# Performance work log

Measured on AMD Instinct MI355X. Metric: run time of the kernel, lower is better.

## Reference

```python
import jax, jax.numpy as jnp
import numpy as np

N_HEADS = 6
N_KV_HEADS = 2
HEAD_DIM = 128
REPEATS = N_HEADS // N_KV_HEADS  # 3


def setup_inputs() -> dict:
    key = jax.random.key(0)
    ks = jax.random.split(key, 5)
    B, S, D = 2, 4096, 768
    std = 1.0 / np.sqrt(D)
    return {
        "x": jax.random.normal(ks[0], (B, S, D), dtype=jnp.float32),
        "wq": jax.random.normal(ks[1], (D, N_HEADS * HEAD_DIM), dtype=jnp.float32) * std,
        "wk": jax.random.normal(ks[2], (D, N_KV_HEADS * HEAD_DIM), dtype=jnp.float32) * std,
        "wv": jax.random.normal(ks[3], (D, N_KV_HEADS * HEAD_DIM), dtype=jnp.float32) * std,
        "wo": jax.random.normal(ks[4], (N_HEADS * HEAD_DIM, D), dtype=jnp.float32) * std,
    }


def reference(x, wq, wk, wv, wo):
    B, S, _ = x.shape
    # projections
    q = (x @ wq).reshape(B, S, N_HEADS, HEAD_DIM)
    k = (x @ wk).reshape(B, S, N_KV_HEADS, HEAD_DIM)
    v = (x @ wv).reshape(B, S, N_KV_HEADS, HEAD_DIM)
    # GQA: repeat kv heads (repeat_interleave along head axis)
    k = jnp.repeat(k, REPEATS, axis=2)  # [B,S,H,D]
    v = jnp.repeat(v, REPEATS, axis=2)
    scale = 1.0 / jnp.sqrt(jnp.asarray(HEAD_DIM, x.dtype))
    # full bidirectional attention, [B,H,S,S] scores
    attn = jnp.einsum("bqhd,bkhd->bhqk", q * scale, k)
    attn = jax.nn.softmax(attn, axis=-1)
    out = jnp.einsum("bhqk,bkhd->bqhd", attn, v).reshape(B, S, N_HEADS * HEAD_DIM)
    return out @ wo
```

## Files before the change

### kernel.cpp

```cpp
#include <hip/hip_runtime.h>


typedef __attribute__((ext_vector_type(8))) short bf16x8;
typedef __attribute__((ext_vector_type(4))) float floatx4;
typedef __attribute__((ext_vector_type(4))) unsigned short ushort4v;

#define MFMA16(a, b, c) __builtin_amdgcn_mfma_f32_16x16x32_bf16((a), (b), (c), 0, 0, 0)

#if __has_builtin(__builtin_amdgcn_exp2f)
#define EXP2F(x) __builtin_amdgcn_exp2f(x)
#else
#define EXP2F(x) exp2f(x)
#endif

#define GLOAD_LDS16(gptr, lptr)                                                   \
  __builtin_amdgcn_global_load_lds(                                               \
      (const __attribute__((address_space(1))) unsigned int*)(gptr),              \
      (__attribute__((address_space(3))) unsigned int*)(lptr), 16, 0, 0)

__device__ __forceinline__ unsigned short f2bf(float f) {
  unsigned int u = __builtin_bit_cast(unsigned int, f);
  u = u + 0x7FFFu + ((u >> 16) & 1u);
  return (unsigned short)(u >> 16);
}

__device__ __forceinline__ unsigned short f2bf_fast(float f) {
  unsigned int u = __builtin_bit_cast(unsigned int, f);
  return (unsigned short)((u + 0x8000u) >> 16);
}

__device__ __forceinline__ float bf2f(unsigned short v) {
  return __builtin_bit_cast(float, (unsigned int)v << 16);
}


__global__ __launch_bounds__(256) void k_cvt_x(const float* __restrict__ x,
                                               unsigned short* __restrict__ xb, int n) {
  int i = (blockIdx.x * 256 + threadIdx.x) * 4;
  if (i + 3 < n) {
    float4 v = *(const float4*)(x + i);
    xb[i + 0] = f2bf(v.x);
    xb[i + 1] = f2bf(v.y);
    xb[i + 2] = f2bf(v.z);
    xb[i + 3] = f2bf(v.w);
  }
}

__global__ __launch_bounds__(256) void k_cvt_w(const float* __restrict__ wq,
                                               const float* __restrict__ wk,
                                               const float* __restrict__ wv,
                                               const float* __restrict__ wo,
                                               unsigned short* __restrict__ wqkvT,
                                               unsigned short* __restrict__ woT) {
  __shared__ float T[64 * 65];
  const float QSCALE = 1.4426950408889634f * 0.08838834764831843f;
  const int kb = blockIdx.x, nb = blockIdx.y, tid = threadIdx.x;

  const float* src; int ld, col0; unsigned short* dst; int n0; float scale = 1.0f;
  if (nb < 12)      { src = wq; ld = 768; col0 = nb * 64;        dst = wqkvT; n0 = nb * 64; scale = QSCALE; }
  else if (nb < 16) { src = wk; ld = 256; col0 = (nb - 12) * 64; dst = wqkvT; n0 = nb * 64; }
  else if (nb < 20) { src = wv; ld = 256; col0 = (nb - 16) * 64; dst = wqkvT; n0 = nb * 64; }
  else              { src = wo; ld = 768; col0 = (nb - 20) * 64; dst = woT;   n0 = (nb - 20) * 64; }

  const int k0 = kb * 64;
  {
    int cc = tid & 63, kk0 = tid >> 6;
#pragma unroll
    for (int it = 0; it < 16; it++) {
      int kk = kk0 + it * 4;
      T[kk * 65 + cc] = src[(size_t)(k0 + kk) * ld + col0 + cc] * scale;
    }
  }
  __syncthreads();
  {
    int kk = tid & 63, nn0 = tid >> 6;
#pragma unroll
    for (int it = 0; it < 16; it++) {
      int nn = nn0 + it * 4;
      dst[(size_t)(n0 + nn) * 768 + k0 + kk] = f2bf(T[kk * 65 + nn]);
    }
  }
}


__device__ __forceinline__ void store_out(float* C, int i, float v) { C[i] = v; }
__device__ __forceinline__ void store_out(unsigned short* C, int i, float v) { C[i] = f2bf(v); }

template <typename OUT_T, bool SPLIT_V>
__global__ __launch_bounds__(256) void k_gemm(const unsigned short* __restrict__ A, int lda,
                                              const unsigned short* __restrict__ Bt, int ldb,
                                              OUT_T* __restrict__ C, int ldc, int K,
                                              unsigned short* __restrict__ vTout) {
  __shared__ __align__(16) unsigned short As0[128 * 32];
  __shared__ __align__(16) unsigned short As1[128 * 32];
  __shared__ __align__(16) unsigned short Bs0[128 * 32];
  __shared__ __align__(16) unsigned short Bs1[128 * 32];

  const int tid = threadIdx.x;
  const int wave = tid >> 6, lane = tid & 63;
  const int quad = lane >> 4, l16 = lane & 15;
  const int wm = (wave >> 1) * 64, wn = (wave & 1) * 64;
  const int m0 = blockIdx.y * 128, n0 = blockIdx.x * 128;

  floatx4 acc[4][4] = {};

  auto stage = [&](const unsigned short* G, int ld, int row0, int k0, unsigned short* S) {
#pragma unroll
    for (int it = 0; it < 2; it++) {
      int j = it * 256 + tid;
      int r = j >> 2, c = (j & 3) ^ (r & 3);
      GLOAD_LDS16((const char*)(G + (size_t)(row0 + r) * ld + k0 + c * 8), &S[j * 8]);
    }
  };

  const int xq = (quad ^ (l16 & 3)) * 8;
  auto compute = [&](const unsigned short* As, const unsigned short* Bs) {
    bf16x8 af[4], bfr[4];
#pragma unroll
    for (int mf = 0; mf < 4; mf++)
      af[mf] = *(const bf16x8*)(&As[(wm + mf * 16 + l16) * 32 + xq]);
#pragma unroll
    for (int nf = 0; nf < 4; nf++)
      bfr[nf] = *(const bf16x8*)(&Bs[(wn + nf * 16 + l16) * 32 + xq]);
#pragma unroll
    for (int mf = 0; mf < 4; mf++)
#pragma unroll
      for (int nf = 0; nf < 4; nf++)
        acc[mf][nf] = MFMA16(af[mf], bfr[nf], acc[mf][nf]);
  };

  stage(A, lda, m0, 0, As0);
  stage(Bt, ldb, n0, 0, Bs0);

  const int half = K >> 6;
#pragma unroll 1
  for (int i = 0; i < half; i++) {
    __syncthreads();
    stage(A, lda, m0, (2 * i + 1) * 32, As1);
    stage(Bt, ldb, n0, (2 * i + 1) * 32, Bs1);
    compute(As0, Bs0);
    __syncthreads();
    if (i < half - 1) {
      stage(A, lda, m0, (2 * i + 2) * 32, As0);
      stage(Bt, ldb, n0, (2 * i + 2) * 32, Bs0);
    }
    compute(As1, Bs1);
  }

#pragma unroll
  for (int mf = 0; mf < 4; mf++)
#pragma unroll
    for (int nf = 0; nf < 4; nf++) {
      int col = n0 + wn + nf * 16 + l16;
      if (SPLIT_V && col >= 1024) {
        int cc = col - 1024;
        int kvhh = cc >> 7, d = cc & 127;
        int row0 = m0 + wm + mf * 16 + quad * 4;
        int bb = row0 >> 12, s = row0 & 4095;
        ushort4v pv;
        pv.x = f2bf(acc[mf][nf][0]);
        pv.y = f2bf(acc[mf][nf][1]);
        pv.z = f2bf(acc[mf][nf][2]);
        pv.w = f2bf(acc[mf][nf][3]);
        *(ushort4v*)(&vTout[((size_t)((bb * 2 + kvhh) * 128) + d) * 4096 + s]) = pv;
      } else {
#pragma unroll
        for (int r = 0; r < 4; r++) {
          int row = m0 + wm + mf * 16 + quad * 4 + r;
          store_out(C, row * ldc + col, acc[mf][nf][r]);
        }
      }
    }
}


#define NSEG 4

#define KS_OFF(row, c) (((row) << 7) + ((((c) ^ ((row) & 7))) << 3))
#define VS_OFF(row, c) (((row) << 6) + ((((c) ^ ((row) & 7))) << 3))

__global__ __launch_bounds__(256) void k_attn(const unsigned short* __restrict__ qkv,
                                              const unsigned short* __restrict__ vT,
                                              unsigned short* __restrict__ Opart,
                                              float* __restrict__ lpart) {
  __shared__ __align__(16) unsigned short Ks[64 * 128];
  __shared__ __align__(16) unsigned short Vt[128 * 64];
  __shared__ __align__(16) unsigned short Ps[128 * 64];

  const int qt = blockIdx.x, h = blockIdx.y;
  const int seg = blockIdx.z >> 1, b = blockIdx.z & 1;
  const int kvh = h / 3;
  const int tid = threadIdx.x, w = tid >> 6, lane = tid & 63;
  const int quad = lane >> 4, l16 = lane & 15;

  const char* qbase = (const char*)(qkv + (size_t)(b * 4096) * 1280 + h * 128);
  const char* kbase = (const char*)(qkv + (size_t)(b * 4096) * 1280 + 768 + kvh * 128);
  const char* vtb   = (const char*)(vT + (size_t)((b * 2 + kvh) * 128) * 4096);

  bf16x8 qf[2][4];
  floatx4 acc[2][8] = {};
  float l_i[2] = {0.f, 0.f};

#pragma unroll
  for (int it = 0; it < 8; it++) {
    int cb = it * 256 + w * 64;
    int j = cb + lane;
    int r = j >> 4, c = (j & 15) ^ (r & 7);
    unsigned short* dst = (cb < 1024) ? &Ks[cb * 8] : &Vt[(cb - 1024) * 8];
    GLOAD_LDS16(qbase + (size_t)(qt * 128 + r) * 2560 + c * 16, dst);
  }
  __syncthreads();

  {
    const unsigned short* qsrc = (w < 2) ? Ks : Vt;
    const int qr0 = (w & 1) * 32;
#pragma unroll
    for (int qg = 0; qg < 2; qg++)
#pragma unroll
      for (int dc = 0; dc < 4; dc++)
        qf[qg][dc] = *(const bf16x8*)(&qsrc[KS_OFF(qr0 + qg * 16 + l16, dc * 4 + quad)]);
  }
  __syncthreads();

  auto stage_k = [&](int kt) {
#pragma unroll
    for (int it = 0; it < 4; it++) {
      int cb = it * 256 + w * 64;
      int j = cb + lane;
      int r = j >> 4, c = (j & 15) ^ (r & 7);
      GLOAD_LDS16(kbase + (size_t)(kt * 64 + r) * 2560 + c * 16, &Ks[cb * 8]);
    }
  };
  auto stage_v = [&](int kt) {
#pragma unroll
    for (int it = 0; it < 4; it++) {
      int cb = it * 256 + w * 64;
      int j = cb + lane;
      int r = j >> 3, c = (j & 7) ^ (r & 7);
      GLOAD_LDS16(vtb + (size_t)r * 8192 + kt * 128 + c * 16, &Vt[cb * 8]);
    }
  };

  const int k0 = seg * 16;
  stage_k(k0);

#pragma unroll 1
  for (int i = 0; i < 16; i++) {
    __syncthreads();
    stage_v(k0 + i);

    floatx4 sfr[2][4] = {};
#pragma unroll
    for (int nf = 0; nf < 4; nf++)
#pragma unroll
      for (int dc = 0; dc < 4; dc++) {
        bf16x8 kf = *(const bf16x8*)(&Ks[KS_OFF(nf * 16 + l16, dc * 4 + quad)]);
        sfr[0][nf] = MFMA16(kf, qf[0][dc], sfr[0][nf]);
        sfr[1][nf] = MFMA16(kf, qf[1][dc], sfr[1][nf]);
      }

#pragma unroll
    for (int qg = 0; qg < 2; qg++) {
      float rs = 0.f;
#pragma unroll
      for (int nf = 0; nf < 4; nf++) {
#pragma unroll
        for (int r = 0; r < 4; r++) {
          float p = EXP2F(sfr[qg][nf][r]);
          sfr[qg][nf][r] = p;
          rs += p;
        }
        int row = w * 32 + qg * 16 + l16;
        int ch = nf * 2 + (quad >> 1);
        ushort4v pw;
        pw.x = f2bf_fast(sfr[qg][nf][0]);
        pw.y = f2bf_fast(sfr[qg][nf][1]);
        pw.z = f2bf_fast(sfr[qg][nf][2]);
        pw.w = f2bf_fast(sfr[qg][nf][3]);
        *(ushort4v*)(&Ps[VS_OFF(row, ch) + (quad & 1) * 4]) = pw;
      }
      rs += __shfl_xor(rs, 16, 64);
      rs += __shfl_xor(rs, 32, 64);
      l_i[qg] += rs;
    }

    __syncthreads();
    if (i < 15) stage_k(k0 + i + 1);

#pragma unroll
    for (int kc = 0; kc < 2; kc++) {
      bf16x8 pf0 = *(const bf16x8*)(&Ps[VS_OFF(w * 32 + l16, kc * 4 + quad)]);
      bf16x8 pf1 = *(const bf16x8*)(&Ps[VS_OFF(w * 32 + 16 + l16, kc * 4 + quad)]);
#pragma unroll
      for (int df = 0; df < 8; df++) {
        bf16x8 vf = *(const bf16x8*)(&Vt[VS_OFF(df * 16 + l16, kc * 4 + quad)]);
        acc[0][df] = MFMA16(pf0, vf, acc[0][df]);
        acc[1][df] = MFMA16(pf1, vf, acc[1][df]);
      }
    }
  }

#pragma unroll
  for (int qg = 0; qg < 2; qg++) {
    if (quad == 0)
      lpart[((size_t)(seg * 2 + b) * 6 + h) * 4096 + qt * 128 + w * 32 + qg * 16 + l16] = l_i[qg];
#pragma unroll
    for (int r = 0; r < 4; r++) {
      int row = qt * 128 + w * 32 + qg * 16 + quad * 4 + r;
      unsigned short* orow =
          Opart + (size_t)seg * 8192 * 768 + (size_t)(b * 4096 + row) * 768 + h * 128;
#pragma unroll
      for (int df = 0; df < 8; df++)
        orow[df * 16 + l16] = f2bf_fast(acc[qg][df][r]);
    }
  }
}

__global__ __launch_bounds__(256) void k_reduce(const unsigned short* __restrict__ Opart,
                                                const float* __restrict__ lpart,
                                                unsigned short* __restrict__ ob) {
  int idx = (blockIdx.x * 256 + threadIdx.x) * 4;
  int row = idx / 768, col = idx - row * 768;
  int h = col >> 7;
  int b = row >> 12, r = row & 4095;

  float lt = 0.f;
#pragma unroll
  for (int s = 0; s < NSEG; s++)
    lt += lpart[((size_t)(s * 2 + b) * 6 + h) * 4096 + r];
  float inv = 1.0f / lt;

  float acc0 = 0.f, acc1 = 0.f, acc2 = 0.f, acc3 = 0.f;
#pragma unroll
  for (int s = 0; s < NSEG; s++) {
    ushort4v v = *(const ushort4v*)(&Opart[(size_t)s * 8192 * 768 + idx]);
    acc0 += bf2f(v.x);
    acc1 += bf2f(v.y);
    acc2 += bf2f(v.z);
    acc3 += bf2f(v.w);
  }
  ushort4v o;
  o.x = f2bf(acc0 * inv);
  o.y = f2bf(acc1 * inv);
  o.z = f2bf(acc2 * inv);
  o.w = f2bf(acc3 * inv);
  *(ushort4v*)(&ob[idx]) = o;
}


extern "C" void kernel_launch(void* const* d_in, const int* in_sizes, int n_in,
                              void* d_out, int out_size, void* d_ws, size_t ws_size,
                              hipStream_t stream) {
  const float* x  = (const float*)d_in[0];
  const float* wq = (const float*)d_in[1];
  const float* wk = (const float*)d_in[2];
  const float* wv = (const float*)d_in[3];
  const float* wo = (const float*)d_in[4];
  float* out = (float*)d_out;

  char* ws = (char*)d_ws;
  unsigned short* xb    = (unsigned short*)(ws);
  unsigned short* wqkvT = (unsigned short*)(ws + 12582912);
  unsigned short* woT   = (unsigned short*)(ws + 14548992);
  unsigned short* qkvb  = (unsigned short*)(ws + 15728640);
  unsigned short* ob    = (unsigned short*)(ws + 36700160);
  unsigned short* Opart = (unsigned short*)(ws + 49283072);
  float*          lpart = (float*)(ws + 99614720);
  unsigned short* vT    = ob;

  k_cvt_x<<<6144, 256, 0, stream>>>(x, xb, 8192 * 768);
  k_cvt_w<<<dim3(12, 32), 256, 0, stream>>>(wq, wk, wv, wo, wqkvT, woT);

  k_gemm<unsigned short, true><<<dim3(10, 64), 256, 0, stream>>>(
      xb, 768, wqkvT, 768, qkvb, 1280, 768, vT);

  k_attn<<<dim3(32, 6, 2 * NSEG), 256, 0, stream>>>(qkvb, vT, Opart, lpart);

  k_reduce<<<6144, 256, 0, stream>>>(Opart, lpart, ob);

  k_gemm<float, false><<<dim3(6, 64), 256, 0, stream>>>(ob, 768, woT, 768, out, 768, 768, nullptr);
}
```

Baseline: 254.5 us.

## Build P operand fragments in registers via lane shuffles instead of LDS

Stops writing the softmax probability tile P to shared memory. The PV MFMA A-operand fragments are now assembled in registers with cross-lane shuffles, and the LDS read-back is gone. Row-sum reduction across lanes moves out of the loop to the epilogue, and launch bounds request 3 blocks per CU. The goal is to cut LDS traffic and LDS footprint so occupancy can rise, at the cost of extra shuffle instructions and register pressure.

```diff
diff --git a/kernel.cpp b/kernel.cpp
--- a/kernel.cpp
+++ b/kernel.cpp
@@ -4,6 +4,7 @@
 typedef __attribute__((ext_vector_type(8))) short bf16x8;
 typedef __attribute__((ext_vector_type(4))) float floatx4;
 typedef __attribute__((ext_vector_type(4))) unsigned short ushort4v;
+typedef __attribute__((ext_vector_type(4))) unsigned int uint4v;
 
 #define MFMA16(a, b, c) __builtin_amdgcn_mfma_f32_16x16x32_bf16((a), (b), (c), 0, 0, 0)
 
@@ -31,6 +32,12 @@
 
 __device__ __forceinline__ float bf2f(unsigned short v) {
   return __builtin_bit_cast(float, (unsigned int)v << 16);
+}
+
+__device__ __forceinline__ unsigned int pack_bf16(float a, float b) {
+  unsigned int ua = __builtin_bit_cast(unsigned int, a);
+  unsigned int ub = __builtin_bit_cast(unsigned int, b);
+  return ((ua + 0x8000u) >> 16) | ((ub + 0x8000u) & 0xFFFF0000u);
 }
 
 
@@ -179,13 +186,12 @@
 #define KS_OFF(row, c) (((row) << 7) + ((((c) ^ ((row) & 7))) << 3))
 #define VS_OFF(row, c) (((row) << 6) + ((((c) ^ ((row) & 7))) << 3))
 
-__global__ __launch_bounds__(256) void k_attn(const unsigned short* __restrict__ qkv,
-                                              const unsigned short* __restrict__ vT,
-                                              unsigned short* __restrict__ Opart,
-                                              float* __restrict__ lpart) {
+__global__ __launch_bounds__(256, 3) void k_attn(const unsigned short* __restrict__ qkv,
+                                                 const unsigned short* __restrict__ vT,
+                                                 unsigned short* __restrict__ Opart,
+                                                 float* __restrict__ lpart) {
   __shared__ __align__(16) unsigned short Ks[64 * 128];
   __shared__ __align__(16) unsigned short Vt[128 * 64];
-  __shared__ __align__(16) unsigned short Ps[128 * 64];
 
   const int qt = blockIdx.x, h = blockIdx.y;
   const int seg = blockIdx.z >> 1, b = blockIdx.z & 1;
@@ -259,29 +265,38 @@
         sfr[1][nf] = MFMA16(kf, qf[1][dc], sfr[1][nf]);
       }
 
+    uint4v frg[2][2];
 #pragma unroll
     for (int qg = 0; qg < 2; qg++) {
       float rs = 0.f;
+      unsigned int pp[4][4];
 #pragma unroll
       for (int nf = 0; nf < 4; nf++) {
-#pragma unroll
-        for (int r = 0; r < 4; r++) {
-          float p = EXP2F(sfr[qg][nf][r]);
-          sfr[qg][nf][r] = p;
-          rs += p;
+        float p0 = EXP2F(sfr[qg][nf][0]);
+        float p1 = EXP2F(sfr[qg][nf][1]);
+        float p2 = EXP2F(sfr[qg][nf][2]);
+        float p3 = EXP2F(sfr[qg][nf][3]);
+        rs += (p0 + p1) + (p2 + p3);
+        unsigned int w0 = pack_bf16(p0, p1);
+        unsigned int w1 = pack_bf16(p2, p3);
+        unsigned int x0 = __shfl_xor(w0, 16, 64);
+        unsigned int x1 = __shfl_xor(w1, 16, 64);
+        bool odd = (quad & 1);
+        pp[nf][0] = odd ? x0 : w0;
+        pp[nf][1] = odd ? x1 : w1;
+        pp[nf][2] = odd ? w0 : x0;
+        pp[nf][3] = odd ? w1 : x1;
+      }
+      l_i[qg] += rs;
+#pragma unroll
+      for (int kc = 0; kc < 2; kc++)
+#pragma unroll
+        for (int u = 0; u < 4; u++) {
+          unsigned int own  = (quad & 1) ? pp[2 * kc + 1][u] : pp[2 * kc][u];
+          unsigned int send = (quad < 2) ? pp[2 * kc + 1][u] : pp[2 * kc][u];
+          unsigned int rcv = __shfl_xor(send, 32, 64);
+          frg[qg][kc][u] = (quad == 0 || quad == 3) ? own : rcv;
         }
-        int row = w * 32 + qg * 16 + l16;
-        int ch = nf * 2 + (quad >> 1);
-        ushort4v pw;
-        pw.x = f2bf_fast(sfr[qg][nf][0]);
-        pw.y = f2bf_fast(sfr[qg][nf][1]);
-        pw.z = f2bf_fast(sfr[qg][nf][2]);
-        pw.w = f2bf_fast(sfr[qg][nf][3]);
-        *(ushort4v*)(&Ps[VS_OFF(row, ch) + (quad & 1) * 4]) = pw;
-      }
-      rs += __shfl_xor(rs, 16, 64);
-      rs += __shfl_xor(rs, 32, 64);
-      l_i[qg] += rs;
     }
 
     __syncthreads();
@@ -289,8 +304,8 @@
 
 #pragma unroll
     for (int kc = 0; kc < 2; kc++) {
-      bf16x8 pf0 = *(const bf16x8*)(&Ps[VS_OFF(w * 32 + l16, kc * 4 + quad)]);
-      bf16x8 pf1 = *(const bf16x8*)(&Ps[VS_OFF(w * 32 + 16 + l16, kc * 4 + quad)]);
+      bf16x8 pf0 = __builtin_bit_cast(bf16x8, frg[0][kc]);
+      bf16x8 pf1 = __builtin_bit_cast(bf16x8, frg[1][kc]);
 #pragma unroll
       for (int df = 0; df < 8; df++) {
         bf16x8 vf = *(const bf16x8*)(&Vt[VS_OFF(df * 16 + l16, kc * 4 + quad)]);
@@ -302,8 +317,11 @@
 
 #pragma unroll
   for (int qg = 0; qg < 2; qg++) {
+    float lt = l_i[qg];
+    lt += __shfl_xor(lt, 16, 64);
+    lt += __shfl_xor(lt, 32, 64);
     if (quad == 0)
-      lpart[((size_t)(seg * 2 + b) * 6 + h) * 4096 + qt * 128 + w * 32 + qg * 16 + l16] = l_i[qg];
+      lpart[((size_t)(seg * 2 + b) * 6 + h) * 4096 + qt * 128 + w * 32 + qg * 16 + l16] = lt;
 #pragma unroll
     for (int r = 0; r < 4; r++) {
       int row = qt * 128 + w * 32 + qg * 16 + quad * 4 + r;
```

Result: slower. 482.1 us (+89.4%).

## Compute softmax row sums via MFMA with ones and split QK into halves with setprio

Applied to the files above, without the earlier changes.

Replaces the per-lane scalar accumulation and cross-lane shuffles for the softmax denominator with an extra MFMA that multiplies the bf16 P tile by a vector of ones. The row sums now come from the rounded bf16 probabilities rather than the fp32 values. The score computation is split into two halves so exp and the P writes of one half can interleave with MFMAs of the other, and s_setprio raises wave priority around the matrix phases. This aims to cut VALU and shuffle work and improve overlap, at the cost of two more MFMAs per chunk and a small numeric difference in the normalizer.

```diff
diff --git a/kernel.cpp b/kernel.cpp
--- a/kernel.cpp
+++ b/kernel.cpp
@@ -199,7 +199,11 @@
 
   bf16x8 qf[2][4];
   floatx4 acc[2][8] = {};
-  float l_i[2] = {0.f, 0.f};
+  floatx4 accl[2] = {};
+
+  bf16x8 onesf;
+#pragma unroll
+  for (int j = 0; j < 8; j++) onesf[j] = (short)0x3F80;
 
 #pragma unroll
   for (int it = 0; it < 8; it++) {
@@ -249,48 +253,51 @@
     __syncthreads();
     stage_v(k0 + i);
 
-    floatx4 sfr[2][4] = {};
-#pragma unroll
-    for (int nf = 0; nf < 4; nf++)
-#pragma unroll
-      for (int dc = 0; dc < 4; dc++) {
-        bf16x8 kf = *(const bf16x8*)(&Ks[KS_OFF(nf * 16 + l16, dc * 4 + quad)]);
-        sfr[0][nf] = MFMA16(kf, qf[0][dc], sfr[0][nf]);
-        sfr[1][nf] = MFMA16(kf, qf[1][dc], sfr[1][nf]);
+#pragma unroll
+    for (int nfh = 0; nfh < 2; nfh++) {
+      floatx4 sfr[2][2] = {};
+      __builtin_amdgcn_s_setprio(1);
+#pragma unroll
+      for (int nfo = 0; nfo < 2; nfo++) {
+        int nf = nfh * 2 + nfo;
+#pragma unroll
+        for (int dc = 0; dc < 4; dc++) {
+          bf16x8 kf = *(const bf16x8*)(&Ks[KS_OFF(nf * 16 + l16, dc * 4 + quad)]);
+          sfr[0][nfo] = MFMA16(kf, qf[0][dc], sfr[0][nfo]);
+          sfr[1][nfo] = MFMA16(kf, qf[1][dc], sfr[1][nfo]);
+        }
       }
-
-#pragma unroll
-    for (int qg = 0; qg < 2; qg++) {
-      float rs = 0.f;
-#pragma unroll
-      for (int nf = 0; nf < 4; nf++) {
-#pragma unroll
-        for (int r = 0; r < 4; r++) {
-          float p = EXP2F(sfr[qg][nf][r]);
-          sfr[qg][nf][r] = p;
-          rs += p;
+      __builtin_amdgcn_s_setprio(0);
+#pragma unroll
+      for (int qg = 0; qg < 2; qg++)
+#pragma unroll
+        for (int nfo = 0; nfo < 2; nfo++) {
+          int nf = nfh * 2 + nfo;
+          float p0 = EXP2F(sfr[qg][nfo][0]);
+          float p1 = EXP2F(sfr[qg][nfo][1]);
+          float p2 = EXP2F(sfr[qg][nfo][2]);
+          float p3 = EXP2F(sfr[qg][nfo][3]);
+          int row = w * 32 + qg * 16 + l16;
+          int ch = nf * 2 + (quad >> 1);
+          ushort4v pw;
+          pw.x = f2bf_fast(p0);
+          pw.y = f2bf_fast(p1);
+          pw.z = f2bf_fast(p2);
+          pw.w = f2bf_fast(p3);
+          *(ushort4v*)(&Ps[VS_OFF(row, ch) + (quad & 1) * 4]) = pw;
         }
-        int row = w * 32 + qg * 16 + l16;
-        int ch = nf * 2 + (quad >> 1);
-        ushort4v pw;
-        pw.x = f2bf_fast(sfr[qg][nf][0]);
-        pw.y = f2bf_fast(sfr[qg][nf][1]);
-        pw.z = f2bf_fast(sfr[qg][nf][2]);
-        pw.w = f2bf_fast(sfr[qg][nf][3]);
-        *(ushort4v*)(&Ps[VS_OFF(row, ch) + (quad & 1) * 4]) = pw;
-      }
-      rs += __shfl_xor(rs, 16, 64);
-      rs += __shfl_xor(rs, 32, 64);
-      l_i[qg] += rs;
     }
 
     __syncthreads();
     if (i < 15) stage_k(k0 + i + 1);
 
+    __builtin_amdgcn_s_setprio(1);
 #pragma unroll
     for (int kc = 0; kc < 2; kc++) {
       bf16x8 pf0 = *(const bf16x8*)(&Ps[VS_OFF(w * 32 + l16, kc * 4 + quad)]);
       bf16x8 pf1 = *(const bf16x8*)(&Ps[VS_OFF(w * 32 + 16 + l16, kc * 4 + quad)]);
+      accl[0] = MFMA16(pf0, onesf, accl[0]);
+      accl[1] = MFMA16(pf1, onesf, accl[1]);
 #pragma unroll
       for (int df = 0; df < 8; df++) {
         bf16x8 vf = *(const bf16x8*)(&Vt[VS_OFF(df * 16 + l16, kc * 4 + quad)]);
@@ -298,12 +305,19 @@
         acc[1][df] = MFMA16(pf1, vf, acc[1][df]);
       }
     }
-  }
-
+    __builtin_amdgcn_s_setprio(0);
+  }
+
+  if (l16 == 0) {
+#pragma unroll
+    for (int qg = 0; qg < 2; qg++)
+#pragma unroll
+      for (int r = 0; r < 4; r++)
+        lpart[((size_t)(seg * 2 + b) * 6 + h) * 4096 + qt * 128 + w * 32 + qg * 16 +
+              quad * 4 + r] = accl[qg][r];
+  }
 #pragma unroll
   for (int qg = 0; qg < 2; qg++) {
-    if (quad == 0)
-      lpart[((size_t)(seg * 2 + b) * 6 + h) * 4096 + qt * 128 + w * 32 + qg * 16 + l16] = l_i[qg];
 #pragma unroll
     for (int r = 0; r < 4; r++) {
       int row = qt * 128 + w * 32 + qg * 16 + quad * 4 + r;
```

Result: no change. 259.2 us (+1.8%).
